# Kernel optimization log

Measured on AMD Instinct MI355X. Metric: run time of the kernel, lower is better.

## Reference

```python
import jax, jax.numpy as jnp
import numpy as np

N = 40000   # nodes
E = 640000  # edges (before self-loops)
G = 64      # graphs
EPS = 1e-5


def _gat_conv(x, src, dst, W, a_src, a_dst, bias, n_nodes):
    """PyG GATConv, heads=1, leaky_relu slope 0.2, with self-loops already in src/dst."""
    h = x @ W.T                              # [N, out]
    s_score = h @ a_src                      # [N]
    d_score = h @ a_dst                      # [N]
    e = jax.nn.leaky_relu(s_score[src] + d_score[dst], 0.2)  # [E]
    m = jax.ops.segment_max(e, dst, num_segments=n_nodes)
    ex = jnp.exp(e - m[dst])
    z = jax.ops.segment_sum(ex, dst, num_segments=n_nodes)
    alpha = ex / z[dst]                      # per-dst softmax over incoming edges
    out = jax.ops.segment_sum(h[src] * alpha[:, None], dst, num_segments=n_nodes)
    return out + bias


def _layer_norm(x, gamma, beta):
    mu = jnp.mean(x, axis=-1, keepdims=True)
    var = jnp.mean((x - mu) ** 2, axis=-1, keepdims=True)
    return gamma * (x - mu) * jax.lax.rsqrt(var + EPS) + beta


def setup_inputs() -> dict:
    key = jax.random.key(0)
    ks = jax.random.split(key, 16)
    x = jax.random.normal(ks[0], (N, 128), dtype=jnp.float32)
    edge_index = jax.random.randint(ks[1], (2, E), 0, N, dtype=jnp.int32)
    batch = jnp.sort(jax.random.randint(ks[2], (N,), 0, G, dtype=jnp.int32))
    def glorot(k, shape):
        fan = shape[-1]
        return jax.random.normal(k, shape, dtype=jnp.float32) / jnp.sqrt(jnp.float32(fan))
    return {
        "x": x, "edge_index": edge_index, "batch": batch,
        "W1": glorot(ks[3], (128, 128)), "a1_src": glorot(ks[4], (128,)),
        "a1_dst": glorot(ks[5], (128,)), "b1": jnp.zeros((128,), jnp.float32),
        "g1": jnp.ones((128,), jnp.float32), "be1": jnp.zeros((128,), jnp.float32),
        "W2": glorot(ks[6], (64, 128)), "a2_src": glorot(ks[7], (64,)),
        "a2_dst": glorot(ks[8], (64,)), "b2": jnp.zeros((64,), jnp.float32),
        "g2": jnp.ones((64,), jnp.float32), "be2": jnp.zeros((64,), jnp.float32),
        "Wl": glorot(ks[9], (64, 64)), "bl": jnp.zeros((64,), jnp.float32),
        "Wc": glorot(ks[10], (1, 64)), "bc": jnp.zeros((1,), jnp.float32),
    }


def reference(x, edge_index, batch, W1, a1_src, a1_dst, b1, g1, be1,
              W2, a2_src, a2_dst, b2, g2, be2, Wl, bl, Wc, bc):
    # add self-loops as PyG GATConv does by default
    loops = jnp.arange(N, dtype=edge_index.dtype)
    src = jnp.concatenate([edge_index[0], loops])
    dst = jnp.concatenate([edge_index[1], loops])

    h = jax.nn.relu(_gat_conv(x, src, dst, W1, a1_src, a1_dst, b1, N))
    h = _layer_norm(h, g1, be1)
    h = jax.nn.relu(_gat_conv(h, src, dst, W2, a2_src, a2_dst, b2, N))
    h = _layer_norm(h, g2, be2)

    # global mean pool over graphs
    sums = jax.ops.segment_sum(h, batch, num_segments=G)          # [G, 64]
    cnt = jax.ops.segment_sum(jnp.ones((N,), h.dtype), batch, num_segments=G)
    pooled = sums / jnp.maximum(cnt, 1.0)[:, None]

    out = pooled @ Wl.T + bl
    out = out @ Wc.T + bc                                          # [G, 1]
    return out.squeeze(-1)                                         # [G]
```

## Files before the change

kernel.cpp:

```cpp
#include <hip/hip_runtime.h>
#include <hip/hip_fp16.h>
#include <math.h>

#define NNODES 40000
#define NEDGES 640000
#define NGRAPH 64
#define CAP 96
constexpr float LN_EPS = 1e-5f;

__device__ __forceinline__ float bf_sum(float v) {
    #pragma unroll
    for (int o = 32; o > 0; o >>= 1) v += __shfl_xor(v, o);
    return v;
}

__global__ void prep(const float* __restrict__ W1, const float* __restrict__ W2,
                     float* __restrict__ Wt1, float* __restrict__ Wt2,
                     int* __restrict__ cnt, float* __restrict__ sums) {
    int t = blockIdx.x * 256 + threadIdx.x;
    if (t < NNODES) cnt[t] = 0;
    if (t < 128 * 128) { int o = t / 128, i = t % 128; Wt1[i * 128 + o] = W1[t]; }
    if (t < 64 * 128)  { int o = t / 128, i = t % 128; Wt2[i * 64 + o] = W2[t]; }
    if (t < NGRAPH * 64) sums[t] = 0.f;
}

__global__ void bin_edges(const int* __restrict__ ei, int E,
                          int* __restrict__ cnt, unsigned short* __restrict__ ssrc) {
    int e = blockIdx.x * blockDim.x + threadIdx.x;
    if (e >= E) return;
    int s = ei[e], d = ei[E + e];
    int pos = atomicAdd(cnt + d, 1);
    if (pos < CAP) ssrc[d * CAP + pos] = (unsigned short)s;
}

template<int DIN, int DOUT, int NPT>
__global__ __launch_bounds__(256) void gemm_scores(
        const float* __restrict__ X, const float* __restrict__ Wt,
        const float* __restrict__ asrc, const float* __restrict__ adst,
        __half* __restrict__ H, float* __restrict__ S, float* __restrict__ Dv) {
    constexpr int CHG = DOUT / 4;
    constexpr int NG  = 256 / CHG;
    constexpr int NPB = NG * NPT;
    static_assert(NPB == 64, "NPB must be 64");
    __shared__ float xs[DIN][NPB];
    __shared__ float ps[NG][NPT][2];
    const int base = blockIdx.x * NPB;
    const int tid = threadIdx.x;
    #pragma unroll
    for (int i4 = tid; i4 < NPB * DIN / 4; i4 += 256) {
        const int nd = i4 % NPB, c4 = i4 / NPB;
        float4 v = *(const float4*)(X + (size_t)(base + nd) * DIN + 4 * c4);
        xs[4 * c4 + 0][nd] = v.x;
        xs[4 * c4 + 1][nd] = v.y;
        xs[4 * c4 + 2][nd] = v.z;
        xs[4 * c4 + 3][nd] = v.w;
    }
    __syncthreads();
    const int cg = tid % CHG, ng = tid / CHG;
    const int c0 = 4 * cg, n0 = ng * NPT;
    float acc[NPT][4];
    #pragma unroll
    for (int n = 0; n < NPT; ++n)
        #pragma unroll
        for (int k = 0; k < 4; ++k) acc[n][k] = 0.f;
    #pragma unroll 2
    for (int i = 0; i < DIN; ++i) {
        const float4 w = *(const float4*)(Wt + i * DOUT + c0);
        #pragma unroll
        for (int n4 = 0; n4 < NPT / 4; ++n4) {
            const float4 xv = *(const float4*)&xs[i][n0 + 4 * n4];
            const float xf[4] = {xv.x, xv.y, xv.z, xv.w};
            #pragma unroll
            for (int j = 0; j < 4; ++j) {
                const int n = 4 * n4 + j;
                acc[n][0] += xf[j] * w.x; acc[n][1] += xf[j] * w.y;
                acc[n][2] += xf[j] * w.z; acc[n][3] += xf[j] * w.w;
            }
        }
    }
    #pragma unroll
    for (int n = 0; n < NPT; ++n) {
        __half2 p01 = __floats2half2_rn(acc[n][0], acc[n][1]);
        __half2 p23 = __floats2half2_rn(acc[n][2], acc[n][3]);
        __half2* hp = (__half2*)(H + (size_t)(base + n0 + n) * DOUT + c0);
        hp[0] = p01; hp[1] = p23;
    }
    const float4 asf = *(const float4*)(asrc + c0);
    const float4 adf = *(const float4*)(adst + c0);
    float sp[NPT], dp[NPT];
    #pragma unroll
    for (int n = 0; n < NPT; ++n) {
        sp[n] = acc[n][0]*asf.x + acc[n][1]*asf.y + acc[n][2]*asf.z + acc[n][3]*asf.w;
        dp[n] = acc[n][0]*adf.x + acc[n][1]*adf.y + acc[n][2]*adf.z + acc[n][3]*adf.w;
    }
    #pragma unroll
    for (int o = CHG / 2; o > 0; o >>= 1) {
        #pragma unroll
        for (int n = 0; n < NPT; ++n) {
            sp[n] += __shfl_xor(sp[n], o);
            dp[n] += __shfl_xor(dp[n], o);
        }
    }
    if (cg == 0) {
        #pragma unroll
        for (int n = 0; n < NPT; ++n) { ps[ng][n][0] = sp[n]; ps[ng][n][1] = dp[n]; }
    }
    __syncthreads();
    if (tid < NPB) {
        S[base + tid]  = ps[tid / NPT][tid % NPT][0];
        Dv[base + tid] = ps[tid / NPT][tid % NPT][1];
    }
}

template<int D, int POOL>
__global__ __launch_bounds__(256) void gat_aggr(
        const int* __restrict__ cnt, const unsigned short* __restrict__ ssrc,
        const float* __restrict__ S, const float* __restrict__ Dv,
        const __half* __restrict__ H,
        const float* __restrict__ b, const float* __restrict__ gam,
        const float* __restrict__ bet,
        float* __restrict__ out, const int* __restrict__ batch,
        float* __restrict__ sums) {
    constexpr int VPL = D / 64;
    const int lane = threadIdx.x & 63;
    const int node = blockIdx.x * 4 + (threadIdx.x >> 6);
    const int deg = min(__builtin_amdgcn_readfirstlane(cnt[node]), CAP);
    const float dsc = Dv[node];
    float ts = S[node] + dsc;
    ts = ts > 0.f ? ts : 0.2f * ts;
    const float aself = __expf(ts);

    float z, acc0 = 0.f, acc1 = 0.f;

    if (deg <= 64) {
        int s = 0; float a = 0.f;
        if (lane < deg) {
            s = ssrc[node * CAP + lane];
            float t = S[s] + dsc;
            t = t > 0.f ? t : 0.2f * t;
            a = __expf(t);
        }
        z = bf_sum(a);
        const int ab = __float_as_int(a);
        const int nmax = (deg + 7) & ~7;
        for (int j = 0; j < nmax; j += 8) {
            float af[8]; __half2 hv[8]; __half hs[8];
            #pragma unroll
            for (int u = 0; u < 8; ++u) {
                const int sj = __builtin_amdgcn_readlane(s, j + u);
                af[u] = __int_as_float(__builtin_amdgcn_readlane(ab, j + u));
                const __half* hp = H + (size_t)sj * D;
                if (VPL == 1) hs[u] = hp[lane];
                else          hv[u] = *(const __half2*)(hp + 2 * lane);
            }
            #pragma unroll
            for (int u = 0; u < 8; ++u) {
                if (VPL == 1) {
                    acc0 += af[u] * __half2float(hs[u]);
                } else {
                    acc0 += af[u] * __half2float(__low2half(hv[u]));
                    acc1 += af[u] * __half2float(__high2half(hv[u]));
                }
            }
        }
    } else {
        float zz = 0.f;
        const int r0 = node * CAP;
        for (int bse = 0; bse < deg; bse += 64) {
            const int n = min(64, deg - bse);
            int s = 0; float a = 0.f;
            if (lane < n) {
                s = ssrc[r0 + bse + lane];
                float t = S[s] + dsc;
                t = t > 0.f ? t : 0.2f * t;
                a = __expf(t);
            }
            zz += bf_sum(a);
            const int abits = __float_as_int(a);
            for (int j = 0; j < n; ++j) {
                const int sj = __builtin_amdgcn_readlane(s, j);
                const float aj = __int_as_float(__builtin_amdgcn_readlane(abits, j));
                const __half* hp = H + (size_t)sj * D;
                if (VPL == 1) {
                    acc0 += aj * __half2float(hp[lane]);
                } else {
                    const float2 f = __half22float2(*(const __half2*)(hp + 2 * lane));
                    acc0 += aj * f.x; acc1 += aj * f.y;
                }
            }
        }
        z = zz;
    }

    {
        const __half* hp = H + (size_t)node * D;
        if (VPL == 1) {
            acc0 += aself * __half2float(hp[lane]);
        } else {
            const float2 f = __half22float2(*(const __half2*)(hp + 2 * lane));
            acc0 += aself * f.x; acc1 += aself * f.y;
        }
        z += aself;
    }

    const float zinv = 1.0f / z;
    float vv[VPL], lsum = 0.f;
    vv[0] = acc0;
    if (VPL == 2) vv[1] = acc1;
    #pragma unroll
    for (int k = 0; k < VPL; ++k) {
        const int ch = VPL * lane + k;
        vv[k] = fmaxf(vv[k] * zinv + b[ch], 0.f);
        lsum += vv[k];
    }
    const float mu = bf_sum(lsum) / D;
    float q = 0.f;
    #pragma unroll
    for (int k = 0; k < VPL; ++k) { vv[k] -= mu; q += vv[k] * vv[k]; }
    const float rstd = rsqrtf(bf_sum(q) / D + LN_EPS);
    #pragma unroll
    for (int k = 0; k < VPL; ++k) {
        const int ch = VPL * lane + k;
        vv[k] = gam[ch] * vv[k] * rstd + bet[ch];
    }
    if (POOL) {
        const int bg = batch[node];
        atomicAdd(&sums[bg * D + lane], vv[0]);
    } else {
        if (VPL == 1) out[(size_t)node * D + lane] = vv[0];
        else *(float2*)(out + (size_t)node * D + 2 * lane) = make_float2(vv[0], vv[1]);
    }
}

__global__ void final_head(const float* __restrict__ sums, const int* __restrict__ batch,
                           const float* __restrict__ Wl, const float* __restrict__ bl,
                           const float* __restrict__ Wc, const float* __restrict__ bc,
                           float* __restrict__ out) {
    __shared__ float p[64];
    __shared__ float red[64];
    const int g = blockIdx.x, tid = threadIdx.x;
    int lo = 0, hi = NNODES;
    while (lo < hi) { int mid = (lo + hi) >> 1; if (batch[mid] < g) lo = mid + 1; else hi = mid; }
    int lo2 = lo, hi2 = NNODES;
    while (lo2 < hi2) { int mid = (lo2 + hi2) >> 1; if (batch[mid] < g + 1) lo2 = mid + 1; else hi2 = mid; }
    const float cnt = (float)(lo2 - lo);
    p[tid] = sums[g * 64 + tid] / fmaxf(cnt, 1.0f);
    __syncthreads();
    float t = bl[tid];
    #pragma unroll 8
    for (int k = 0; k < 64; ++k) t += Wl[tid * 64 + k] * p[k];
    red[tid] = Wc[tid] * t;
    __syncthreads();
    for (int s = 32; s > 0; s >>= 1) {
        if (tid < s) red[tid] += red[tid + s];
        __syncthreads();
    }
    if (tid == 0) out[g] = red[0] + bc[0];
}

extern "C" void kernel_launch(void* const* d_in, const int* in_sizes, int n_in,
                              void* d_out, int out_size, void* d_ws, size_t ws_size,
                              hipStream_t stream) {
    const int N = NNODES, E = NEDGES, G = NGRAPH;

    const float* x      = (const float*)d_in[0];
    const int*   ei     = (const int*)d_in[1];
    const int*   batch  = (const int*)d_in[2];
    const float* W1     = (const float*)d_in[3];
    const float* a1s    = (const float*)d_in[4];
    const float* a1d    = (const float*)d_in[5];
    const float* b1     = (const float*)d_in[6];
    const float* g1     = (const float*)d_in[7];
    const float* be1    = (const float*)d_in[8];
    const float* W2     = (const float*)d_in[9];
    const float* a2s    = (const float*)d_in[10];
    const float* a2d    = (const float*)d_in[11];
    const float* b2     = (const float*)d_in[12];
    const float* g2     = (const float*)d_in[13];
    const float* be2    = (const float*)d_in[14];
    const float* Wl     = (const float*)d_in[15];
    const float* bl     = (const float*)d_in[16];
    const float* Wc     = (const float*)d_in[17];
    const float* bc     = (const float*)d_in[18];

    char* w = (char*)d_ws;
    __half* h1  = (__half*)w; w += (size_t)N * 128 * 2;
    float* acc1 = (float*)w; w += (size_t)N * 128 * 4;
    float* S    = (float*)w; w += (size_t)N * 4;
    float* Dv   = (float*)w; w += (size_t)N * 4;
    int* cnt    = (int*)w;   w += (size_t)N * 4;
    unsigned short* ssrc = (unsigned short*)w; w += (size_t)N * CAP * 2;
    float* Wt1  = (float*)w; w += (size_t)128 * 128 * 4;
    float* Wt2  = (float*)w; w += (size_t)128 * 64 * 4;
    float* sums = (float*)w; w += (size_t)G * 64 * 4;
    __half* h2 = h1;

    const int TB = 256;
    const int gridN = (N + 255) / 256;

    prep<<<gridN, 256, 0, stream>>>(W1, W2, Wt1, Wt2, cnt, sums);

    bin_edges<<<(E + TB - 1) / TB, TB, 0, stream>>>(ei, E, cnt, ssrc);

    gemm_scores<128, 128, 8><<<N / 64, 256, 0, stream>>>(x, Wt1, a1s, a1d, h1, S, Dv);
    gat_aggr<128, 0><<<N / 4, 256, 0, stream>>>(cnt, ssrc, S, Dv, h1, b1, g1, be1,
                                                acc1, nullptr, nullptr);

    gemm_scores<128, 64, 4><<<N / 64, 256, 0, stream>>>(acc1, Wt2, a2s, a2d, h2, S, Dv);
    gat_aggr<64, 1><<<N / 4, 256, 0, stream>>>(cnt, ssrc, S, Dv, h2, b2, g2, be2,
                                               nullptr, batch, sums);

    final_head<<<G, 64, 0, stream>>>(sums, batch, Wl, bl, Wc, bc, (float*)d_out);
}
```

Measured before the change: 275.6 us.

## Use fp16 packed dot2 in node GEMMs and merge edge binning with first GEMM

The node-feature GEMMs now pre-pack the transposed weights and the staged inputs as fp16 pairs and accumulate with the packed fdot2 instruction into fp32. This halves LDS and weight traffic and the number of FMA instructions. Separately, the edge-binning kernel is merged into the first GEMM launch as extra blocks, so the atomic binning can overlap with the GEMM and one launch disappears. The cost is reduced input precision, since x and W are rounded to fp16 before the multiply.

```diff
diff --git a/kernel.cpp b/kernel.cpp
--- a/kernel.cpp
+++ b/kernel.cpp
@@ -6,7 +6,24 @@
 #define NEDGES 640000
 #define NGRAPH 64
 #define CAP 96
+#define BIN_BLOCKS ((NEDGES + 255) / 256)
 constexpr float LN_EPS = 1e-5f;
+
+typedef _Float16 half2_t __attribute__((ext_vector_type(2)));
+
+#if defined(__has_builtin)
+#if __has_builtin(__builtin_amdgcn_fdot2)
+#define HAS_FDOT2 1
+#endif
+#endif
+
+__device__ __forceinline__ float dot2acc(half2_t x, half2_t w, float acc) {
+#ifdef HAS_FDOT2
+    return __builtin_amdgcn_fdot2(x, w, acc, false);
+#else
+    return acc + (float)x.x * (float)w.x + (float)x.y * (float)w.y;
+#endif
+}
 
 __device__ __forceinline__ float bf_sum(float v) {
     #pragma unroll
@@ -15,45 +32,45 @@
 }
 
 __global__ void prep(const float* __restrict__ W1, const float* __restrict__ W2,
-                     float* __restrict__ Wt1, float* __restrict__ Wt2,
+                     unsigned* __restrict__ Wth1, unsigned* __restrict__ Wth2,
                      int* __restrict__ cnt, float* __restrict__ sums) {
     int t = blockIdx.x * 256 + threadIdx.x;
     if (t < NNODES) cnt[t] = 0;
-    if (t < 128 * 128) { int o = t / 128, i = t % 128; Wt1[i * 128 + o] = W1[t]; }
-    if (t < 64 * 128)  { int o = t / 128, i = t % 128; Wt2[i * 64 + o] = W2[t]; }
+    if (t < 64 * 128) {
+        int i2 = t / 128, o = t % 128;
+        half2_t h = { (_Float16)W1[o * 128 + 2 * i2], (_Float16)W1[o * 128 + 2 * i2 + 1] };
+        Wth1[i2 * 128 + o] = __builtin_bit_cast(unsigned, h);
+    }
+    if (t < 64 * 64) {
+        int i2 = t / 64, o = t % 64;
+        half2_t h = { (_Float16)W2[o * 128 + 2 * i2], (_Float16)W2[o * 128 + 2 * i2 + 1] };
+        Wth2[i2 * 64 + o] = __builtin_bit_cast(unsigned, h);
+    }
     if (t < NGRAPH * 64) sums[t] = 0.f;
 }
 
-__global__ void bin_edges(const int* __restrict__ ei, int E,
-                          int* __restrict__ cnt, unsigned short* __restrict__ ssrc) {
-    int e = blockIdx.x * blockDim.x + threadIdx.x;
-    if (e >= E) return;
-    int s = ei[e], d = ei[E + e];
-    int pos = atomicAdd(cnt + d, 1);
-    if (pos < CAP) ssrc[d * CAP + pos] = (unsigned short)s;
-}
-
 template<int DIN, int DOUT, int NPT>
-__global__ __launch_bounds__(256) void gemm_scores(
-        const float* __restrict__ X, const float* __restrict__ Wt,
+__device__ __forceinline__ void gemm_body(
+        int gb, const float* __restrict__ X, const unsigned* __restrict__ Wth,
         const float* __restrict__ asrc, const float* __restrict__ adst,
-        __half* __restrict__ H, float* __restrict__ S, float* __restrict__ Dv) {
+        __half* __restrict__ H, float* __restrict__ S, float* __restrict__ Dv,
+        unsigned* xsu ,
+        float* psf   ) {
     constexpr int CHG = DOUT / 4;
     constexpr int NG  = 256 / CHG;
-    constexpr int NPB = NG * NPT;
-    static_assert(NPB == 64, "NPB must be 64");
-    __shared__ float xs[DIN][NPB];
-    __shared__ float ps[NG][NPT][2];
-    const int base = blockIdx.x * NPB;
+    constexpr int NPB = 64;
+    constexpr int K2  = DIN / 2;
+    static_assert(NG * NPT == NPB, "grid math");
+    const int base = gb * NPB;
     const int tid = threadIdx.x;
     #pragma unroll
     for (int i4 = tid; i4 < NPB * DIN / 4; i4 += 256) {
         const int nd = i4 % NPB, c4 = i4 / NPB;
         float4 v = *(const float4*)(X + (size_t)(base + nd) * DIN + 4 * c4);
-        xs[4 * c4 + 0][nd] = v.x;
-        xs[4 * c4 + 1][nd] = v.y;
-        xs[4 * c4 + 2][nd] = v.z;
-        xs[4 * c4 + 3][nd] = v.w;
+        half2_t a = { (_Float16)v.x, (_Float16)v.y };
+        half2_t b = { (_Float16)v.z, (_Float16)v.w };
+        xsu[(2 * c4 + 0) * NPB + nd] = __builtin_bit_cast(unsigned, a);
+        xsu[(2 * c4 + 1) * NPB + nd] = __builtin_bit_cast(unsigned, b);
     }
     __syncthreads();
     const int cg = tid % CHG, ng = tid / CHG;
@@ -64,26 +81,31 @@
         #pragma unroll
         for (int k = 0; k < 4; ++k) acc[n][k] = 0.f;
     #pragma unroll 2
-    for (int i = 0; i < DIN; ++i) {
-        const float4 w = *(const float4*)(Wt + i * DOUT + c0);
+    for (int i2 = 0; i2 < K2; ++i2) {
+        const uint4 wu = *(const uint4*)(Wth + i2 * DOUT + c0);
+        half2_t w[4] = { __builtin_bit_cast(half2_t, wu.x), __builtin_bit_cast(half2_t, wu.y),
+                         __builtin_bit_cast(half2_t, wu.z), __builtin_bit_cast(half2_t, wu.w) };
         #pragma unroll
         for (int n4 = 0; n4 < NPT / 4; ++n4) {
-            const float4 xv = *(const float4*)&xs[i][n0 + 4 * n4];
-            const float xf[4] = {xv.x, xv.y, xv.z, xv.w};
+            const uint4 xu = *(const uint4*)(xsu + i2 * NPB + n0 + 4 * n4);
+            half2_t x[4] = { __builtin_bit_cast(half2_t, xu.x), __builtin_bit_cast(half2_t, xu.y),
+                             __builtin_bit_cast(half2_t, xu.z), __builtin_bit_cast(half2_t, xu.w) };
             #pragma unroll
             for (int j = 0; j < 4; ++j) {
                 const int n = 4 * n4 + j;
-                acc[n][0] += xf[j] * w.x; acc[n][1] += xf[j] * w.y;
-                acc[n][2] += xf[j] * w.z; acc[n][3] += xf[j] * w.w;
+                acc[n][0] = dot2acc(x[j], w[0], acc[n][0]);
+                acc[n][1] = dot2acc(x[j], w[1], acc[n][1]);
+                acc[n][2] = dot2acc(x[j], w[2], acc[n][2]);
+                acc[n][3] = dot2acc(x[j], w[3], acc[n][3]);
             }
         }
     }
     #pragma unroll
     for (int n = 0; n < NPT; ++n) {
-        __half2 p01 = __floats2half2_rn(acc[n][0], acc[n][1]);
-        __half2 p23 = __floats2half2_rn(acc[n][2], acc[n][3]);
-        __half2* hp = (__half2*)(H + (size_t)(base + n0 + n) * DOUT + c0);
-        hp[0] = p01; hp[1] = p23;
+        half2_t p01 = { (_Float16)acc[n][0], (_Float16)acc[n][1] };
+        half2_t p23 = { (_Float16)acc[n][2], (_Float16)acc[n][3] };
+        uint2 pk = { __builtin_bit_cast(unsigned, p01), __builtin_bit_cast(unsigned, p23) };
+        *(uint2*)(H + (size_t)(base + n0 + n) * DOUT + c0) = pk;
     }
     const float4 asf = *(const float4*)(asrc + c0);
     const float4 adf = *(const float4*)(adst + c0);
@@ -103,13 +125,46 @@
     }
     if (cg == 0) {
         #pragma unroll
-        for (int n = 0; n < NPT; ++n) { ps[ng][n][0] = sp[n]; ps[ng][n][1] = dp[n]; }
+        for (int n = 0; n < NPT; ++n) {
+            psf[(ng * NPT + n) * 2 + 0] = sp[n];
+            psf[(ng * NPT + n) * 2 + 1] = dp[n];
+        }
     }
     __syncthreads();
     if (tid < NPB) {
-        S[base + tid]  = ps[tid / NPT][tid % NPT][0];
-        Dv[base + tid] = ps[tid / NPT][tid % NPT][1];
-    }
+        S[base + tid]  = psf[tid * 2 + 0];
+        Dv[base + tid] = psf[tid * 2 + 1];
+    }
+}
+
+__global__ __launch_bounds__(256) void bin_gemm1(
+        const int* __restrict__ ei,
+        int* __restrict__ cnt, unsigned short* __restrict__ ssrc,
+        const float* __restrict__ X, const unsigned* __restrict__ Wth1,
+        const float* __restrict__ a1s, const float* __restrict__ a1d,
+        __half* __restrict__ H, float* __restrict__ S, float* __restrict__ Dv) {
+    __shared__ unsigned xsu[64 * 64];
+    __shared__ float psf[64 * 2];
+    if (blockIdx.x < BIN_BLOCKS) {
+        int e = blockIdx.x * 256 + threadIdx.x;
+        if (e < NEDGES) {
+            int s = ei[e], d = ei[NEDGES + e];
+            int pos = atomicAdd(cnt + d, 1);
+            if (pos < CAP) ssrc[d * CAP + pos] = (unsigned short)s;
+        }
+    } else {
+        gemm_body<128, 128, 8>(blockIdx.x - BIN_BLOCKS, X, Wth1, a1s, a1d,
+                               H, S, Dv, xsu, psf);
+    }
+}
+
+__global__ __launch_bounds__(256) void gemm2_k(
+        const float* __restrict__ X, const unsigned* __restrict__ Wth2,
+        const float* __restrict__ a2s, const float* __restrict__ a2d,
+        __half* __restrict__ H, float* __restrict__ S, float* __restrict__ Dv) {
+    __shared__ unsigned xsu[64 * 64];
+    __shared__ float psf[64 * 2];
+    gemm_body<128, 64, 4>(blockIdx.x, X, Wth2, a2s, a2d, H, S, Dv, xsu, psf);
 }
 
 template<int D, int POOL>
@@ -261,7 +316,7 @@
 extern "C" void kernel_launch(void* const* d_in, const int* in_sizes, int n_in,
                               void* d_out, int out_size, void* d_ws, size_t ws_size,
                               hipStream_t stream) {
-    const int N = NNODES, E = NEDGES, G = NGRAPH;
+    const int N = NNODES, G = NGRAPH;
 
     const float* x      = (const float*)d_in[0];
     const int*   ei     = (const int*)d_in[1];
@@ -290,23 +345,22 @@
     float* Dv   = (float*)w; w += (size_t)N * 4;
     int* cnt    = (int*)w;   w += (size_t)N * 4;
     unsigned short* ssrc = (unsigned short*)w; w += (size_t)N * CAP * 2;
-    float* Wt1  = (float*)w; w += (size_t)128 * 128 * 4;
-    float* Wt2  = (float*)w; w += (size_t)128 * 64 * 4;
+    unsigned* Wth1 = (unsigned*)w; w += (size_t)64 * 128 * 4;
+    unsigned* Wth2 = (unsigned*)w; w += (size_t)64 * 64 * 4;
     float* sums = (float*)w; w += (size_t)G * 64 * 4;
     __half* h2 = h1;
 
-    const int TB = 256;
     const int gridN = (N + 255) / 256;
 
-    prep<<<gridN, 256, 0, stream>>>(W1, W2, Wt1, Wt2, cnt, sums);
-
-    bin_edges<<<(E + TB - 1) / TB, TB, 0, stream>>>(ei, E, cnt, ssrc);
-
-    gemm_scores<128, 128, 8><<<N / 64, 256, 0, stream>>>(x, Wt1, a1s, a1d, h1, S, Dv);
+    prep<<<gridN, 256, 0, stream>>>(W1, W2, Wth1, Wth2, cnt, sums);
+
+    bin_gemm1<<<BIN_BLOCKS + N / 64, 256, 0, stream>>>(
+        ei, cnt, ssrc, x, Wth1, a1s, a1d, h1, S, Dv);
+
     gat_aggr<128, 0><<<N / 4, 256, 0, stream>>>(cnt, ssrc, S, Dv, h1, b1, g1, be1,
                                                 acc1, nullptr, nullptr);
 
-    gemm_scores<128, 64, 4><<<N / 64, 256, 0, stream>>>(acc1, Wt2, a2s, a2d, h2, S, Dv);
+    gemm2_k<<<N / 64, 256, 0, stream>>>(acc1, Wth2, a2s, a2d, h2, S, Dv);
     gat_aggr<64, 1><<<N / 4, 256, 0, stream>>>(cnt, ssrc, S, Dv, h2, b2, g2, be2,
                                                nullptr, batch, sums);
 
```

New measurement: 279.2 us. About the same (+1.3%).
